# Kernel tuning notes

Measured on AMD Instinct MI355X. Metric: run time of the kernel, lower is better.

Reference implementation:

```python
import jax, jax.numpy as jnp
import numpy as np
import math

H = 16
D_MODEL = 1024
B, S = 2, 2048

def setup_inputs() -> dict:
    key = jax.random.key(0)
    ks = jax.random.split(key, 7)
    q = jax.random.normal(ks[0], (B, S, D_MODEL), dtype=jnp.float32)
    k = jax.random.normal(ks[1], (B, S, D_MODEL), dtype=jnp.float32)
    v = jax.random.normal(ks[2], (B, S, D_MODEL), dtype=jnp.float32)
    mask = jnp.ones((1, 1, S, S), dtype=jnp.int32)
    sc = 1.0 / math.sqrt(D_MODEL)
    W_Q = jax.random.normal(ks[3], (D_MODEL, D_MODEL), dtype=jnp.float32) * sc
    W_K = jax.random.normal(ks[4], (D_MODEL, D_MODEL), dtype=jnp.float32) * sc
    W_V = jax.random.normal(ks[5], (D_MODEL, D_MODEL), dtype=jnp.float32) * sc
    W_T = jax.random.normal(ks[6], (D_MODEL, D_MODEL), dtype=jnp.float32) * sc
    return {"q": q, "k": k, "v": v, "mask": mask, "W_Q": W_Q, "W_K": W_K, "W_V": W_V, "W_T": W_T}

def reference(q, k, v, mask, W_Q, W_K, W_V, W_T):
    # W matrices stored as (in, out); nn.Linear applies x @ W.T with W (out,in),
    # equivalent here since we treat these directly as projection matrices.
    def split_heads(x):  # [B,S,D] -> [B,H,S,hd]
        Bq, Sq, Dq = x.shape
        return x.reshape(Bq, Sq, H, Dq // H).transpose(0, 2, 1, 3)

    Q = split_heads(q @ W_Q)
    K = split_heads(k @ W_K)
    V = split_heads(v @ W_V)
    d_k = Q.shape[-1]
    score = jnp.einsum("bhqd,bhkd->bhqk", Q, K) / math.sqrt(d_k)
    score = jnp.where(mask == 0, jnp.float32(-1e9), score)
    attn = jax.nn.softmax(score, axis=-1)
    out = jnp.einsum("bhqk,bhkd->bhqd", attn, V)
    out = out.transpose(0, 2, 1, 3).reshape(q.shape[0], q.shape[1], D_MODEL)
    return out @ W_T
```

## Files before the change

kernel.cpp:

```cpp
#include <hip/hip_runtime.h>
#include <hip/hip_bf16.h>
#include <stdint.h>

#define H  16
#define DM 1024
#define BB 2
#define SS 2048
#define HD 64

#define QSCALE 0.18033688011112042f
#define MASKVAL -57.7078f

typedef __attribute__((ext_vector_type(8))) short bf16x8;
typedef __attribute__((ext_vector_type(4))) float f32x4;

__device__ __forceinline__ short f2bf(float f) {
  __hip_bfloat16 h = __float2bfloat16(f);
  return *reinterpret_cast<short*>(&h);
}

__device__ __forceinline__ void load16_lds(const short* g, short* l) {
  __builtin_amdgcn_global_load_lds(
      (const __attribute__((address_space(1))) void*)g,
      (__attribute__((address_space(3))) void*)l, 16, 0, 0);
}

__global__ void transpose_w_kernel(const float* __restrict__ Wq, const float* __restrict__ Wk,
                                   const float* __restrict__ Wv, const float* __restrict__ Wt,
                                   short* __restrict__ dst) {
  __shared__ short tile[32][33];
  int z = blockIdx.z;
  const float* src = (z == 0) ? Wq : (z == 1) ? Wk : (z == 2) ? Wv : Wt;
  short* out = dst + (size_t)z * DM * DM;
  int c0 = blockIdx.x * 32, r0 = blockIdx.y * 32;
  int tx = threadIdx.x, ty = threadIdx.y;
  for (int j = 0; j < 4; j++)
    tile[ty + j * 8][tx] = f2bf(src[(size_t)(r0 + ty + j * 8) * DM + c0 + tx]);
  __syncthreads();
  for (int j = 0; j < 4; j++)
    out[(size_t)(c0 + ty + j * 8) * DM + r0 + tx] = tile[tx][ty + j * 8];
}

__global__ void transpose_v_kernel(const short* __restrict__ Vbuf, short* __restrict__ Vt) {
  __shared__ short tile[32][33];
  int bh = blockIdx.z;
  int s0 = blockIdx.x * 32, d0 = blockIdx.y * 32;
  int tx = threadIdx.x, ty = threadIdx.y;
  for (int j = 0; j < 4; j++)
    tile[ty + j * 8][tx] = Vbuf[((size_t)bh * SS + s0 + ty + j * 8) * HD + d0 + tx];
  __syncthreads();
  for (int j = 0; j < 4; j++)
    Vt[((size_t)bh * HD + d0 + ty + j * 8) * SS + s0 + tx] = tile[tx][ty + j * 8];
}

__global__ void convert_bf16_kernel(const float* __restrict__ q, const float* __restrict__ k,
                                    const float* __restrict__ v, short* __restrict__ dst) {
  int z = blockIdx.z;
  const float* src = (z == 0) ? q : (z == 1) ? k : v;
  short* out = dst + (size_t)z * BB * SS * DM;
  size_t i = ((size_t)blockIdx.x * blockDim.x + threadIdx.x) * 4;
  float4 f = *(const float4*)&src[i];
  short tmp[4] = {f2bf(f.x), f2bf(f.y), f2bf(f.z), f2bf(f.w)};
  *(int2*)&out[i] = *(const int2*)tmp;
}

__global__ void flag_init_kernel(int* flag) { if (threadIdx.x < 2) flag[threadIdx.x] = 0; }

__global__ void mask_scan_kernel(const int4* __restrict__ mask4, int n4, int* __restrict__ flag) {
  int idx = blockIdx.x * blockDim.x + threadIdx.x;
  int stride = gridDim.x * blockDim.x;
  int any = 0;
  for (int i = idx; i < n4; i += stride) {
    int4 m = mask4[i];
    if (m.x == 0 || m.y == 0 || m.z == 0 || m.w == 0) any = 1;
  }
  if (any) atomicOr(flag, 1);
}

__global__ void signal_fill_kernel(float* __restrict__ out, int n) {
  int i = blockIdx.x * blockDim.x + threadIdx.x;
  if (i < n) out[i] = 1.0f;
}

template <int AF32>
__device__ __forceinline__ void gemm_fast_body(const void* __restrict__ Av,
                                               const short* __restrict__ Bt,
                                               void* __restrict__ Cv, int mode, float scale) {
  __shared__ __align__(16) short As[128 * 32];
  __shared__ __align__(16) short Bs[128 * 32];
  int m0 = blockIdx.x * 128, n0 = blockIdx.y * 128;
  int t = threadIdx.x;
  int lane = t & 63, w = t >> 6;
  int l16 = lane & 15, quad = lane >> 4;
  int wm = (w >> 1) * 64, wn = (w & 1) * 64;
  f32x4 acc[4][4] = {};

  for (int k0 = 0; k0 < DM; k0 += 32) {
    if (AF32) {
      const float* A = (const float*)Av;
      for (int i = 0; i < 4; i++) {
        int c = t + i * 256;
        int row = c >> 3, seg = c & 7;
        float4 f = *(const float4*)&A[(size_t)(m0 + row) * DM + k0 + seg * 4];
        short tmp[4] = {f2bf(f.x), f2bf(f.y), f2bf(f.z), f2bf(f.w)};
        *(int2*)&As[row * 32 + seg * 4] = *(const int2*)tmp;
      }
    } else {
      const short* A = (const short*)Av;
      for (int i = 0; i < 2; i++) {
        int c = t + i * 256;
        load16_lds(&A[(size_t)(m0 + (c >> 2)) * DM + k0 + (c & 3) * 8], &As[c * 8]);
      }
    }
    for (int i = 0; i < 2; i++) {
      int c = t + i * 256;
      load16_lds(&Bt[(size_t)(n0 + (c >> 2)) * DM + k0 + (c & 3) * 8], &Bs[c * 8]);
    }
    __syncthreads();
    bf16x8 af[4], bfr[4];
    for (int i = 0; i < 4; i++) af[i]  = *(const bf16x8*)&As[(wm + i * 16 + l16) * 32 + quad * 8];
    for (int i = 0; i < 4; i++) bfr[i] = *(const bf16x8*)&Bs[(wn + i * 16 + l16) * 32 + quad * 8];
    for (int mi = 0; mi < 4; mi++)
      for (int ni = 0; ni < 4; ni++)
        acc[mi][ni] = __builtin_amdgcn_mfma_f32_16x16x32_bf16(af[mi], bfr[ni], acc[mi][ni], 0, 0, 0);
    __syncthreads();
  }

  for (int mi = 0; mi < 4; mi++)
    for (int ni = 0; ni < 4; ni++)
      for (int r = 0; r < 4; r++) {
        int m = m0 + wm + mi * 16 + quad * 4 + r;
        int n = n0 + wn + ni * 16 + l16;
        if (mode == 0) {
          short* C = (short*)Cv;
          int b = m >> 11, s = m & (SS - 1);
          int h = n >> 6, d = n & (HD - 1);
          C[(((size_t)(b * H + h) * SS) + s) * HD + d] = f2bf(acc[mi][ni][r] * scale);
        } else {
          float* C = (float*)Cv;
          C[(size_t)m * DM + n] = acc[mi][ni][r];
        }
      }
}

template <int AF32>
__global__ __launch_bounds__(256, 2) void gemm_qkv_fast_kernel(
    const void* __restrict__ A0, const void* __restrict__ A1, const void* __restrict__ A2,
    const short* __restrict__ WTall,
    short* __restrict__ Qb, short* __restrict__ Kb, short* __restrict__ Vb) {
  int z = blockIdx.z;
  const void* A = (z == 0) ? A0 : (z == 1) ? A1 : A2;
  const short* B = WTall + (size_t)z * DM * DM;
  short* C = (z == 0) ? Qb : (z == 1) ? Kb : Vb;
  gemm_fast_body<AF32>(A, B, (void*)C, 0, (z == 0) ? QSCALE : 1.0f);
}

__global__ __launch_bounds__(256, 2) void gemm_out_fast_kernel(
    const short* __restrict__ Obuf, const short* __restrict__ WtT, float* __restrict__ out) {
  gemm_fast_body<0>((const void*)Obuf, WtT, (void*)out, 2, 1.0f);
}

#define LDT 40
#define LDB 136

template <int AF32>
__device__ __forceinline__ void gemm_legacy_body(const void* __restrict__ Av,
                                                 const float* __restrict__ Bm,
                                                 void* __restrict__ Cv, int mode, float scale) {
  __shared__ __align__(16) short As[128 * LDT];
  __shared__ __align__(16) short Bsh[32 * LDB];
  int m0 = blockIdx.x * 128, n0 = blockIdx.y * 128;
  int t = threadIdx.x;
  int lane = t & 63, w = t >> 6;
  int l16 = lane & 15, quad = lane >> 4;
  int wm = (w >> 1) * 64, wn = (w & 1) * 64;
  f32x4 acc[4][4] = {};

  for (int k0 = 0; k0 < DM; k0 += 32) {
    if (AF32) {
      const float* A = (const float*)Av;
      for (int i = 0; i < 4; i++) {
        int c = t + i * 256;
        int row = c >> 3, seg = c & 7;
        float4 f = *(const float4*)&A[(size_t)(m0 + row) * DM + k0 + seg * 4];
        short tmp[4] = {f2bf(f.x), f2bf(f.y), f2bf(f.z), f2bf(f.w)};
        *(int2*)&As[row * LDT + seg * 4] = *(const int2*)tmp;
      }
    } else {
      const short* A = (const short*)Av;
      for (int i = 0; i < 2; i++) {
        int c = t + i * 256;
        int row = c >> 2, seg = c & 3;
        *(int4*)&As[row * LDT + seg * 8] = *(const int4*)&A[(size_t)(m0 + row) * DM + k0 + seg * 8];
      }
    }
    for (int i = 0; i < 4; i++) {
      int c = t + i * 256;
      int krow = c >> 5, nseg = c & 31;
      float4 f = *(const float4*)&Bm[(size_t)(k0 + krow) * DM + n0 + nseg * 4];
      short tmp[4] = {f2bf(f.x), f2bf(f.y), f2bf(f.z), f2bf(f.w)};
      *(int2*)&Bsh[krow * LDB + nseg * 4] = *(const int2*)tmp;
    }
    __syncthreads();
    bf16x8 af[4], bfr[4];
    for (int i = 0; i < 4; i++) af[i] = *(const bf16x8*)&As[(wm + i * 16 + l16) * LDT + quad * 8];
    for (int i = 0; i < 4; i++) {
      bf16x8 tmp;
      for (int j = 0; j < 8; j++) tmp[j] = Bsh[(quad * 8 + j) * LDB + wn + i * 16 + l16];
      bfr[i] = tmp;
    }
    for (int mi = 0; mi < 4; mi++)
      for (int ni = 0; ni < 4; ni++)
        acc[mi][ni] = __builtin_amdgcn_mfma_f32_16x16x32_bf16(af[mi], bfr[ni], acc[mi][ni], 0, 0, 0);
    __syncthreads();
  }

  for (int mi = 0; mi < 4; mi++)
    for (int ni = 0; ni < 4; ni++)
      for (int r = 0; r < 4; r++) {
        int m = m0 + wm + mi * 16 + quad * 4 + r;
        int n = n0 + wn + ni * 16 + l16;
        if (mode == 0) {
          short* C = (short*)Cv;
          int b = m >> 11, s = m & (SS - 1);
          int h = n >> 6, d = n & (HD - 1);
          C[(((size_t)(b * H + h) * SS) + s) * HD + d] = f2bf(acc[mi][ni][r] * scale);
        } else {
          float* C = (float*)Cv;
          C[(size_t)m * DM + n] = acc[mi][ni][r];
        }
      }
}

__global__ __launch_bounds__(256, 2) void gemm_qkv_legacy_kernel(
    const float* __restrict__ q, const float* __restrict__ k, const float* __restrict__ v,
    const float* __restrict__ B0, const float* __restrict__ B1, const float* __restrict__ B2,
    short* __restrict__ Qb, short* __restrict__ Kb, short* __restrict__ Vb) {
  int z = blockIdx.z;
  const float* A = (z == 0) ? q : (z == 1) ? k : v;
  const float* B = (z == 0) ? B0 : (z == 1) ? B1 : B2;
  short* C = (z == 0) ? Qb : (z == 1) ? Kb : Vb;
  gemm_legacy_body<1>((const void*)A, B, (void*)C, 0, (z == 0) ? QSCALE : 1.0f);
}

__global__ __launch_bounds__(256, 2) void gemm_out_legacy_kernel(
    const short* __restrict__ Obuf, const float* __restrict__ Wt, float* __restrict__ out) {
  gemm_legacy_body<0>((const void*)Obuf, Wt, (void*)out, 2, 1.0f);
}

#define LDP 72

template <int VT>
__global__ __launch_bounds__(256, 4) void attn_kernel(
    const short* __restrict__ Q, const short* __restrict__ K,
    const short* __restrict__ V, const int* __restrict__ mask,
    const int* __restrict__ flag, short* __restrict__ O) {
  __shared__ __align__(16) short Ks[64 * 64];
  __shared__ __align__(16) short Vs[64 * 64];
  __shared__ __align__(16) short Ps[4][16 * LDP];

  int bh = blockIdx.y;
  int q0 = blockIdx.x * 64;
  int t = threadIdx.x, lane = t & 63, w = t >> 6;
  int l16 = lane & 15, quad = lane >> 4;
  int use_mask = flag[0];

  const short* qrow = Q + ((size_t)bh * SS + q0 + w * 16 + l16) * HD;
  bf16x8 aq0 = *(const bf16x8*)&qrow[quad * 8];
  bf16x8 aq1 = *(const bf16x8*)&qrow[32 + quad * 8];

  float lsum[4] = {0.f, 0.f, 0.f, 0.f};
  f32x4 oacc[4] = {};

  const short* Kbase = K + (size_t)bh * SS * HD;
  const short* Vbase = VT ? (V + (size_t)bh * HD * SS)
                          : (V + (size_t)bh * SS * HD);
  int dd = t & 63, h2 = t >> 6;

  for (int kt = 0; kt < SS / 64; kt++) {
    int kb = kt * 64;
    for (int i = 0; i < 2; i++) {
      int p = t + i * 256;
      int rp = p >> 3, cp = p & 7;
      int lc = cp ^ (rp & 7);
      load16_lds(&Kbase[(size_t)(kb + rp) * HD + lc * 8], &Ks[p * 8]);
    }
    if (VT) {
      for (int i = 0; i < 2; i++) {
        int p = t + i * 256;
        int rp = p >> 3, cp = p & 7;
        int lc = cp ^ (rp & 7);
        load16_lds(&Vbase[(size_t)rp * SS + kb + lc * 8], &Vs[p * 8]);
      }
    } else {
      for (int sgi = 0; sgi < 2; sgi++) {
        int sg = h2 * 2 + sgi;
        short tmp[8];
        for (int jj = 0; jj < 8; jj++)
          tmp[jj] = Vbase[(size_t)(kb + sg * 8 + jj) * HD + dd];
        *(int4*)&Vs[dd * 64 + ((sg ^ (dd & 7)) * 8)] = *(const int4*)tmp;
      }
    }
    __syncthreads();

    for (int nb = 0; nb < 4; nb++) {
      f32x4 sc = {};
      bf16x8 bk0 = *(const bf16x8*)&Ks[(nb * 16 + l16) * 64 + ((quad ^ (l16 & 7)) * 8)];
      bf16x8 bk1 = *(const bf16x8*)&Ks[(nb * 16 + l16) * 64 + (((quad + 4) ^ (l16 & 7)) * 8)];
      sc = __builtin_amdgcn_mfma_f32_16x16x32_bf16(aq0, bk0, sc, 0, 0, 0);
      sc = __builtin_amdgcn_mfma_f32_16x16x32_bf16(aq1, bk1, sc, 0, 0, 0);
      if (use_mask) {
        int kg = kb + nb * 16 + l16;
        for (int r = 0; r < 4; r++) {
          int qg = q0 + w * 16 + quad * 4 + r;
          if (mask[(size_t)qg * SS + kg] == 0) sc[r] = MASKVAL;
        }
      }
      for (int r = 0; r < 4; r++) {
        float pv = __builtin_exp2f(fminf(sc[r], 115.0f));
        lsum[r] += pv;
        Ps[w][(quad * 4 + r) * LDP + nb * 16 + l16] = f2bf(pv);
      }
    }

    for (int c = 0; c < 2; c++) {
      bf16x8 ap = *(const bf16x8*)&Ps[w][l16 * LDP + c * 32 + quad * 8];
      for (int nb2 = 0; nb2 < 4; nb2++) {
        bf16x8 bv = *(const bf16x8*)&Vs[(nb2 * 16 + l16) * 64 + (((c * 4 + quad) ^ (l16 & 7)) * 8)];
        oacc[nb2] = __builtin_amdgcn_mfma_f32_16x16x32_bf16(ap, bv, oacc[nb2], 0, 0, 0);
      }
    }
    __syncthreads();
  }

  for (int st = 1; st < 16; st <<= 1)
    for (int r = 0; r < 4; r++) lsum[r] += __shfl_xor(lsum[r], st);

  int b = bh >> 4, h = bh & 15;
  for (int r = 0; r < 4; r++) {
    float inv = 1.0f / lsum[r];
    int qg = q0 + w * 16 + quad * 4 + r;
    for (int nb2 = 0; nb2 < 4; nb2++) {
      int d = nb2 * 16 + l16;
      O[((size_t)(b * SS + qg)) * DM + h * HD + d] = f2bf(oacc[nb2][r] * inv);
    }
  }
}

extern "C" void kernel_launch(void* const* d_in, const int* in_sizes, int n_in,
                              void* d_out, int out_size, void* d_ws, size_t ws_size,
                              hipStream_t stream) {
  const float* q    = (const float*)d_in[0];
  const float* k    = (const float*)d_in[1];
  const float* v    = (const float*)d_in[2];
  const int*   mask = (const int*)d_in[3];
  const float* Wq   = (const float*)d_in[4];
  const float* Wk   = (const float*)d_in[5];
  const float* Wv   = (const float*)d_in[6];
  const float* Wt   = (const float*)d_in[7];
  float* out = (float*)d_out;

  char* ws = (char*)d_ws;
  const size_t MB = 1024ull * 1024ull;
  const size_t NEED_A = 66 * MB;
  const size_t NEED_B = 40 * MB + 4096;
  const size_t NEED_C = 32 * MB + 4096;

  if (ws_size >= NEED_B) {
    short* WTall = (short*)(ws);
    short* Qbuf  = (short*)(ws + 8 * MB);
    short* Kbuf  = (short*)(ws + 16 * MB);
    short* Vbuf  = (short*)(ws + 24 * MB);
    short* Obuf  = (short*)(ws + 32 * MB);
    int*   flag  = (int*)(ws + 40 * MB);

    flag_init_kernel<<<1, 64, 0, stream>>>(flag);
    mask_scan_kernel<<<512, 256, 0, stream>>>((const int4*)mask, SS * SS / 4, flag);
    transpose_w_kernel<<<dim3(32, 32, 4), dim3(32, 8), 0, stream>>>(Wq, Wk, Wv, Wt, WTall);
    if (ws_size >= NEED_A) {
      short* Abf = (short*)(ws + 41 * MB);
      short* Vt  = Abf;
      convert_bf16_kernel<<<dim3(4096, 1, 3), 256, 0, stream>>>(q, k, v, Abf);
      gemm_qkv_fast_kernel<0><<<dim3(BB * SS / 128, DM / 128, 3), 256, 0, stream>>>(
          Abf, Abf + (size_t)BB * SS * DM, Abf + 2ull * BB * SS * DM, WTall, Qbuf, Kbuf, Vbuf);
      transpose_v_kernel<<<dim3(SS / 32, HD / 32, BB * H), dim3(32, 8), 0, stream>>>(Vbuf, Vt);
      attn_kernel<1><<<dim3(SS / 64, BB * H), 256, 0, stream>>>(Qbuf, Kbuf, Vt, mask, flag, Obuf);
    } else {
      gemm_qkv_fast_kernel<1><<<dim3(BB * SS / 128, DM / 128, 3), 256, 0, stream>>>(
          q, k, v, WTall, Qbuf, Kbuf, Vbuf);
      attn_kernel<0><<<dim3(SS / 64, BB * H), 256, 0, stream>>>(Qbuf, Kbuf, Vbuf, mask, flag, Obuf);
    }
    gemm_out_fast_kernel<<<dim3(BB * SS / 128, DM / 128), 256, 0, stream>>>(
        Obuf, WTall + 3ull * DM * DM, out);
  } else if (ws_size >= NEED_C) {
    short* Qbuf = (short*)(ws);
    short* Kbuf = (short*)(ws + 8 * MB);
    short* Vbuf = (short*)(ws + 16 * MB);
    short* Obuf = (short*)(ws + 24 * MB);
    int*   flag = (int*)(ws + 32 * MB);

    flag_init_kernel<<<1, 64, 0, stream>>>(flag);
    mask_scan_kernel<<<512, 256, 0, stream>>>((const int4*)mask, SS * SS / 4, flag);
    gemm_qkv_legacy_kernel<<<dim3(BB * SS / 128, DM / 128, 3), 256, 0, stream>>>(
        q, k, v, Wq, Wk, Wv, Qbuf, Kbuf, Vbuf);
    attn_kernel<0><<<dim3(SS / 64, BB * H), 256, 0, stream>>>(Qbuf, Kbuf, Vbuf, mask, flag, Obuf);
    gemm_out_legacy_kernel<<<dim3(BB * SS / 128, DM / 128), 256, 0, stream>>>(Obuf, Wt, out);
  } else {
    signal_fill_kernel<<<(BB * SS * DM + 255) / 256, 256, 0, stream>>>(out, BB * SS * DM);
  }
}
```

Before: 266.3 us.

## Use 128-query attention tiles and fold flag init and mask scan into prep kernels

Adds an attention kernel in which each block handles 128 queries and each wave processes two 16-row query groups. Each K/V tile loaded into LDS is then reused by twice as many queries, and the K fragments are shared across both groups. The QK product uses swapped operands so scores come out transposed, and Ps is sized to match. Flag initialisation moves into the weight transpose kernel and the mask scan into the bf16 conversion kernel (using an atomicOr), which removes two launches. In exchange the grid halves to 512 blocks, register pressure rises, and launch bounds drop to 2 blocks per SM.

```diff
diff --git a/kernel.cpp b/kernel.cpp
--- a/kernel.cpp
+++ b/kernel.cpp
@@ -27,7 +27,9 @@
 
 __global__ void transpose_w_kernel(const float* __restrict__ Wq, const float* __restrict__ Wk,
                                    const float* __restrict__ Wv, const float* __restrict__ Wt,
-                                   short* __restrict__ dst) {
+                                   short* __restrict__ dst, int* __restrict__ flag) {
+  if (blockIdx.x == 0 && blockIdx.y == 0 && blockIdx.z == 0 &&
+      threadIdx.y == 0 && threadIdx.x < 2) flag[threadIdx.x] = 0;
   __shared__ short tile[32][33];
   int z = blockIdx.z;
   const float* src = (z == 0) ? Wq : (z == 1) ? Wk : (z == 2) ? Wv : Wt;
@@ -53,9 +55,16 @@
     Vt[((size_t)bh * HD + d0 + ty + j * 8) * SS + s0 + tx] = tile[tx][ty + j * 8];
 }
 
-__global__ void convert_bf16_kernel(const float* __restrict__ q, const float* __restrict__ k,
-                                    const float* __restrict__ v, short* __restrict__ dst) {
+__global__ void convert_mask_kernel(const float* __restrict__ q, const float* __restrict__ k,
+                                    const float* __restrict__ v, short* __restrict__ dst,
+                                    const int4* __restrict__ mask4, int* __restrict__ flag) {
   int z = blockIdx.z;
+  if (z == 3) {
+    int idx = blockIdx.x * blockDim.x + threadIdx.x;
+    int4 m = mask4[idx];
+    if (m.x == 0 || m.y == 0 || m.z == 0 || m.w == 0) atomicOr(flag, 1);
+    return;
+  }
   const float* src = (z == 0) ? q : (z == 1) ? k : v;
   short* out = dst + (size_t)z * BB * SS * DM;
   size_t i = ((size_t)blockIdx.x * blockDim.x + threadIdx.x) * 4;
@@ -250,32 +259,32 @@
 
 #define LDP 72
 
-template <int VT>
-__global__ __launch_bounds__(256, 4) void attn_kernel(
+__global__ __launch_bounds__(256, 2) void attn128_kernel(
     const short* __restrict__ Q, const short* __restrict__ K,
-    const short* __restrict__ V, const int* __restrict__ mask,
+    const short* __restrict__ Vt, const int* __restrict__ mask,
     const int* __restrict__ flag, short* __restrict__ O) {
   __shared__ __align__(16) short Ks[64 * 64];
   __shared__ __align__(16) short Vs[64 * 64];
-  __shared__ __align__(16) short Ps[4][16 * LDP];
+  __shared__ __align__(16) short Ps[4][32 * LDP];
 
   int bh = blockIdx.y;
-  int q0 = blockIdx.x * 64;
+  int q0 = blockIdx.x * 128;
   int t = threadIdx.x, lane = t & 63, w = t >> 6;
   int l16 = lane & 15, quad = lane >> 4;
   int use_mask = flag[0];
 
-  const short* qrow = Q + ((size_t)bh * SS + q0 + w * 16 + l16) * HD;
-  bf16x8 aq0 = *(const bf16x8*)&qrow[quad * 8];
-  bf16x8 aq1 = *(const bf16x8*)&qrow[32 + quad * 8];
-
-  float lsum[4] = {0.f, 0.f, 0.f, 0.f};
-  f32x4 oacc[4] = {};
-
-  const short* Kbase = K + (size_t)bh * SS * HD;
-  const short* Vbase = VT ? (V + (size_t)bh * HD * SS)
-                          : (V + (size_t)bh * SS * HD);
-  int dd = t & 63, h2 = t >> 6;
+  bf16x8 aq[2][2];
+  for (int g = 0; g < 2; g++) {
+    const short* qrow = Q + ((size_t)bh * SS + q0 + w * 32 + g * 16 + l16) * HD;
+    aq[g][0] = *(const bf16x8*)&qrow[quad * 8];
+    aq[g][1] = *(const bf16x8*)&qrow[32 + quad * 8];
+  }
+
+  float lsum[2] = {0.f, 0.f};
+  f32x4 oacc[2][4] = {};
+
+  const short* Kbase = K  + (size_t)bh * SS * HD;
+  const short* Vbase = Vt + (size_t)bh * HD * SS;
 
   for (int kt = 0; kt < SS / 64; kt++) {
     int kb = kt * 64;
@@ -284,22 +293,106 @@
       int rp = p >> 3, cp = p & 7;
       int lc = cp ^ (rp & 7);
       load16_lds(&Kbase[(size_t)(kb + rp) * HD + lc * 8], &Ks[p * 8]);
-    }
-    if (VT) {
-      for (int i = 0; i < 2; i++) {
-        int p = t + i * 256;
-        int rp = p >> 3, cp = p & 7;
-        int lc = cp ^ (rp & 7);
-        load16_lds(&Vbase[(size_t)rp * SS + kb + lc * 8], &Vs[p * 8]);
-      }
-    } else {
-      for (int sgi = 0; sgi < 2; sgi++) {
-        int sg = h2 * 2 + sgi;
-        short tmp[8];
-        for (int jj = 0; jj < 8; jj++)
-          tmp[jj] = Vbase[(size_t)(kb + sg * 8 + jj) * HD + dd];
-        *(int4*)&Vs[dd * 64 + ((sg ^ (dd & 7)) * 8)] = *(const int4*)tmp;
-      }
+      load16_lds(&Vbase[(size_t)rp * SS + kb + lc * 8], &Vs[p * 8]);
+    }
+    __syncthreads();
+
+    for (int kb2 = 0; kb2 < 4; kb2++) {
+      int krow = kb2 * 16 + l16;
+      bf16x8 k0 = *(const bf16x8*)&Ks[krow * 64 + ((quad ^ (l16 & 7)) * 8)];
+      bf16x8 k1 = *(const bf16x8*)&Ks[krow * 64 + (((quad + 4) ^ (l16 & 7)) * 8)];
+      for (int g = 0; g < 2; g++) {
+        f32x4 sc = {};
+        sc = __builtin_amdgcn_mfma_f32_16x16x32_bf16(k0, aq[g][0], sc, 0, 0, 0);
+        sc = __builtin_amdgcn_mfma_f32_16x16x32_bf16(k1, aq[g][1], sc, 0, 0, 0);
+        if (use_mask) {
+          int qg = q0 + w * 32 + g * 16 + l16;
+          for (int r = 0; r < 4; r++) {
+            int kg = kb + kb2 * 16 + quad * 4 + r;
+            if (mask[(size_t)qg * SS + kg] == 0) sc[r] = MASKVAL;
+          }
+        }
+        float pv[4];
+        for (int r = 0; r < 4; r++) {
+          pv[r] = __builtin_exp2f(fminf(sc[r], 115.0f));
+          lsum[g] += pv[r];
+        }
+        unsigned u0 = ((unsigned)(unsigned short)f2bf(pv[1]) << 16) | (unsigned short)f2bf(pv[0]);
+        unsigned u1 = ((unsigned)(unsigned short)f2bf(pv[3]) << 16) | (unsigned short)f2bf(pv[2]);
+        uint2 packed = {u0, u1};
+        *(uint2*)&Ps[w][(g * 16 + l16) * LDP + kb2 * 16 + quad * 4] = packed;
+      }
+    }
+
+    for (int c = 0; c < 2; c++) {
+      bf16x8 ap[2];
+      for (int g = 0; g < 2; g++)
+        ap[g] = *(const bf16x8*)&Ps[w][(g * 16 + l16) * LDP + c * 32 + quad * 8];
+      for (int nb2 = 0; nb2 < 4; nb2++) {
+        bf16x8 bv = *(const bf16x8*)&Vs[(nb2 * 16 + l16) * 64 + (((c * 4 + quad) ^ (l16 & 7)) * 8)];
+        for (int g = 0; g < 2; g++)
+          oacc[g][nb2] = __builtin_amdgcn_mfma_f32_16x16x32_bf16(ap[g], bv, oacc[g][nb2], 0, 0, 0);
+      }
+    }
+    __syncthreads();
+  }
+
+  for (int g = 0; g < 2; g++) {
+    lsum[g] += __shfl_xor(lsum[g], 16);
+    lsum[g] += __shfl_xor(lsum[g], 32);
+  }
+
+  int b = bh >> 4, h = bh & 15;
+  for (int g = 0; g < 2; g++)
+    for (int r = 0; r < 4; r++) {
+      float inv = 1.0f / __shfl(lsum[g], quad * 4 + r);
+      int qg = q0 + w * 32 + g * 16 + quad * 4 + r;
+      for (int nb2 = 0; nb2 < 4; nb2++) {
+        int d = nb2 * 16 + l16;
+        O[((size_t)(b * SS + qg)) * DM + h * HD + d] = f2bf(oacc[g][nb2][r] * inv);
+      }
+    }
+}
+
+__global__ __launch_bounds__(256, 4) void attn64_kernel(
+    const short* __restrict__ Q, const short* __restrict__ K,
+    const short* __restrict__ V, const int* __restrict__ mask,
+    const int* __restrict__ flag, short* __restrict__ O) {
+  __shared__ __align__(16) short Ks[64 * 64];
+  __shared__ __align__(16) short Vs[64 * 64];
+  __shared__ __align__(16) short Ps[4][16 * LDP];
+
+  int bh = blockIdx.y;
+  int q0 = blockIdx.x * 64;
+  int t = threadIdx.x, lane = t & 63, w = t >> 6;
+  int l16 = lane & 15, quad = lane >> 4;
+  int use_mask = flag[0];
+
+  const short* qrow = Q + ((size_t)bh * SS + q0 + w * 16 + l16) * HD;
+  bf16x8 aq0 = *(const bf16x8*)&qrow[quad * 8];
+  bf16x8 aq1 = *(const bf16x8*)&qrow[32 + quad * 8];
+
+  float lsum[4] = {0.f, 0.f, 0.f, 0.f};
+  f32x4 oacc[4] = {};
+
+  const short* Kbase = K + (size_t)bh * SS * HD;
+  const short* Vbase = V + (size_t)bh * SS * HD;
+  int dd = t & 63, h2 = t >> 6;
+
+  for (int kt = 0; kt < SS / 64; kt++) {
+    int kb = kt * 64;
+    for (int i = 0; i < 2; i++) {
+      int p = t + i * 256;
+      int rp = p >> 3, cp = p & 7;
+      int lc = cp ^ (rp & 7);
+      load16_lds(&Kbase[(size_t)(kb + rp) * HD + lc * 8], &Ks[p * 8]);
+    }
+    for (int sgi = 0; sgi < 2; sgi++) {
+      int sg = h2 * 2 + sgi;
+      short tmp[8];
+      for (int jj = 0; jj < 8; jj++)
+        tmp[jj] = Vbase[(size_t)(kb + sg * 8 + jj) * HD + dd];
+      *(int4*)&Vs[dd * 64 + ((sg ^ (dd & 7)) * 8)] = *(const int4*)tmp;
     }
     __syncthreads();
 
@@ -366,30 +459,37 @@
   const size_t NEED_B = 40 * MB + 4096;
   const size_t NEED_C = 32 * MB + 4096;
 
-  if (ws_size >= NEED_B) {
+  if (ws_size >= NEED_A) {
     short* WTall = (short*)(ws);
     short* Qbuf  = (short*)(ws + 8 * MB);
     short* Kbuf  = (short*)(ws + 16 * MB);
     short* Vbuf  = (short*)(ws + 24 * MB);
     short* Obuf  = (short*)(ws + 32 * MB);
     int*   flag  = (int*)(ws + 40 * MB);
-
-    flag_init_kernel<<<1, 64, 0, stream>>>(flag);
+    short* Abf   = (short*)(ws + 41 * MB);
+    short* Vt    = Abf;
+
+    transpose_w_kernel<<<dim3(32, 32, 4), dim3(32, 8), 0, stream>>>(Wq, Wk, Wv, Wt, WTall, flag);
+    convert_mask_kernel<<<dim3(4096, 1, 4), 256, 0, stream>>>(q, k, v, Abf, (const int4*)mask, flag);
+    gemm_qkv_fast_kernel<0><<<dim3(BB * SS / 128, DM / 128, 3), 256, 0, stream>>>(
+        Abf, Abf + (size_t)BB * SS * DM, Abf + 2ull * BB * SS * DM, WTall, Qbuf, Kbuf, Vbuf);
+    transpose_v_kernel<<<dim3(SS / 32, HD / 32, BB * H), dim3(32, 8), 0, stream>>>(Vbuf, Vt);
+    attn128_kernel<<<dim3(SS / 128, BB * H), 256, 0, stream>>>(Qbuf, Kbuf, Vt, mask, flag, Obuf);
+    gemm_out_fast_kernel<<<dim3(BB * SS / 128, DM / 128), 256, 0, stream>>>(
+        Obuf, WTall + 3ull * DM * DM, out);
+  } else if (ws_size >= NEED_B) {
+    short* WTall = (short*)(ws);
+    short* Qbuf  = (short*)(ws + 8 * MB);
+    short* Kbuf  = (short*)(ws + 16 * MB);
+    short* Vbuf  = (short*)(ws + 24 * MB);
+    short* Obuf  = (short*)(ws + 32 * MB);
+    int*   flag  = (int*)(ws + 40 * MB);
+
+    transpose_w_kernel<<<dim3(32, 32, 4), dim3(32, 8), 0, stream>>>(Wq, Wk, Wv, Wt, WTall, flag);
     mask_scan_kernel<<<512, 256, 0, stream>>>((const int4*)mask, SS * SS / 4, flag);
-    transpose_w_kernel<<<dim3(32, 32, 4), dim3(32, 8), 0, stream>>>(Wq, Wk, Wv, Wt, WTall);
-    if (ws_size >= NEED_A) {
-      short* Abf = (short*)(ws + 41 * MB);
-      short* Vt  = Abf;
-      convert_bf16_kernel<<<dim3(4096, 1, 3), 256, 0, stream>>>(q, k, v, Abf);
-      gemm_qkv_fast_kernel<0><<<dim3(BB * SS / 128, DM / 128, 3), 256, 0, stream>>>(
-          Abf, Abf + (size_t)BB * SS * DM, Abf + 2ull * BB * SS * DM, WTall, Qbuf, Kbuf, Vbuf);
-      transpose_v_kernel<<<dim3(SS / 32, HD / 32, BB * H), dim3(32, 8), 0, stream>>>(Vbuf, Vt);
-      attn_kernel<1><<<dim3(SS / 64, BB * H), 256, 0, stream>>>(Qbuf, Kbuf, Vt, mask, flag, Obuf);
-    } else {
-      gemm_qkv_fast_kernel<1><<<dim3(BB * SS / 128, DM / 128, 3), 256, 0, stream>>>(
-          q, k, v, WTall, Qbuf, Kbuf, Vbuf);
-      attn_kernel<0><<<dim3(SS / 64, BB * H), 256, 0, stream>>>(Qbuf, Kbuf, Vbuf, mask, flag, Obuf);
-    }
+    gemm_qkv_fast_kernel<1><<<dim3(BB * SS / 128, DM / 128, 3), 256, 0, stream>>>(
+        q, k, v, WTall, Qbuf, Kbuf, Vbuf);
+    attn64_kernel<<<dim3(SS / 64, BB * H), 256, 0, stream>>>(Qbuf, Kbuf, Vbuf, mask, flag, Obuf);
     gemm_out_fast_kernel<<<dim3(BB * SS / 128, DM / 128), 256, 0, stream>>>(
         Obuf, WTall + 3ull * DM * DM, out);
   } else if (ws_size >= NEED_C) {
@@ -403,7 +503,7 @@
     mask_scan_kernel<<<512, 256, 0, stream>>>((const int4*)mask, SS * SS / 4, flag);
     gemm_qkv_legacy_kernel<<<dim3(BB * SS / 128, DM / 128, 3), 256, 0, stream>>>(
         q, k, v, Wq, Wk, Wv, Qbuf, Kbuf, Vbuf);
-    attn_kernel<0><<<dim3(SS / 64, BB * H), 256, 0, stream>>>(Qbuf, Kbuf, Vbuf, mask, flag, Obuf);
+    attn64_kernel<<<dim3(SS / 64, BB * H), 256, 0, stream>>>(Qbuf, Kbuf, Vbuf, mask, flag, Obuf);
     gemm_out_legacy_kernel<<<dim3(BB * SS / 128, DM / 128), 256, 0, stream>>>(Obuf, Wt, out);
   } else {
     signal_fill_kernel<<<(BB * SS * DM + 255) / 256, 256, 0, stream>>>(out, BB * SS * DM);
```

New measurement: 265.5 us. Within noise of the previous version (-0.3%).
